# Optimization experiments

Measured on AMD Instinct MI355X. Metric: run time of the kernel, lower is better.

## Reference

```python
import jax, jax.numpy as jnp
import numpy as np

N_NODES = 50000
N_EDGES = 800000
IN_CH = 128
HID = 64
HEADS = 2
OUT_CH = 64
NEG_SLOPE = 0.2  # PyG GATv2Conv default


def setup_inputs() -> dict:
    key = jax.random.key(0)
    ks = jax.random.split(key, 16)
    x = jax.random.normal(ks[0], (N_NODES, IN_CH), dtype=jnp.float32)
    edge_index = jax.random.randint(ks[1], (2, N_EDGES), 0, N_NODES, dtype=jnp.int64)

    def glorot(k, shape):
        fan_in = shape[0]
        return jax.random.normal(k, shape, dtype=jnp.float32) / np.float32(np.sqrt(fan_in))

    # layer 1: in=128 -> heads=2, ch=64 (concat -> 128)
    # layer 2: in=128 -> heads=2, ch=64 (concat -> 128)
    # layer 3: in=128 -> heads=1, ch=64
    return {
        "x": x,
        "edge_index": edge_index,
        "W1l": glorot(ks[2], (IN_CH, HEADS * HID)),
        "W1r": glorot(ks[3], (IN_CH, HEADS * HID)),
        "att1": glorot(ks[4], (HEADS, HID)),
        "b1": jnp.zeros((HEADS * HID,), jnp.float32),
        "W2l": glorot(ks[5], (HEADS * HID, HEADS * HID)),
        "W2r": glorot(ks[6], (HEADS * HID, HEADS * HID)),
        "att2": glorot(ks[7], (HEADS, HID)),
        "b2": jnp.zeros((HEADS * HID,), jnp.float32),
        "W3l": glorot(ks[8], (HEADS * HID, OUT_CH)),
        "W3r": glorot(ks[9], (HEADS * HID, OUT_CH)),
        "att3": glorot(ks[10], (1, OUT_CH)),
        "b3": jnp.zeros((OUT_CH,), jnp.float32),
    }


def gatv2_conv(x, src, dst, Wl, Wr, att, bias, heads, ch):
    """One GATv2Conv layer (concat=True, self-loops already in src/dst)."""
    n = x.shape[0]
    xl = (x @ Wl).reshape(n, heads, ch)  # source-side transform (messages)
    xr = (x @ Wr).reshape(n, heads, ch)  # target-side transform
    # edge-wise GATv2 scoring: a^T LeakyReLU(xl_j + xr_i)
    e = jax.nn.leaky_relu(xl[src] + xr[dst], NEG_SLOPE)      # [E, H, C]
    logits = jnp.einsum('ehc,hc->eh', e, att)                 # [E, H]
    # segment softmax over incoming edges of each destination node
    amax = jax.ops.segment_max(logits, dst, num_segments=n)   # [N, H]
    ex = jnp.exp(logits - amax[dst])
    denom = jax.ops.segment_sum(ex, dst, num_segments=n)
    alpha = ex / denom[dst]                                   # [E, H]
    out = jax.ops.segment_sum(xl[src] * alpha[:, :, None], dst, num_segments=n)
    return out.reshape(n, heads * ch) + bias


def reference(x, edge_index, W1l, W1r, att1, b1, W2l, W2r, att2, b2, W3l, W3r, att3, b3):
    n = x.shape[0]
    loops = jnp.arange(n, dtype=edge_index.dtype)
    src = jnp.concatenate([edge_index[0], loops])  # add_self_loops=True
    dst = jnp.concatenate([edge_index[1], loops])
    h = jax.nn.elu(gatv2_conv(x, src, dst, W1l, W1r, att1, b1, HEADS, HID))
    h = jax.nn.elu(gatv2_conv(h, src, dst, W2l, W2r, att2, b2, HEADS, HID))
    h = jax.nn.elu(gatv2_conv(h, src, dst, W3l, W3r, att3, b3, 1, OUT_CH))
    return h
```

## Files before the change

### kernel.cpp

```cpp
#include <hip/hip_runtime.h>
#include <hip/hip_fp16.h>
#include <math.h>

#define N_NODES 50000
#define N_EDGES 800000
#define NEG_SLOPE 0.2f

#define BKT_SHIFT 7
#define N_BKT 512
#define NB_CSR ((N_NODES + 127) / 128)
#define CHUNK 2048
#define BCAP 4096
#define PB_CAP 4096
#define G1_BLOCKS (((N_NODES + 127) / 128) * 2)

typedef _Float16 v8h __attribute__((ext_vector_type(8)));
typedef _Float16 h4  __attribute__((ext_vector_type(4)));
typedef _Float16 h2  __attribute__((ext_vector_type(2)));
typedef float f32x4 __attribute__((ext_vector_type(4)));
typedef float f32x2 __attribute__((ext_vector_type(2)));

static inline int cdiv(long long a, int b) { return (int)((a + b - 1) / b); }

template<int CTRL>
static __device__ __forceinline__ float dpp_xadd(float s) {
    int t = __builtin_amdgcn_mov_dpp(__builtin_bit_cast(int, s), CTRL, 0xf, 0xf, true);
    return s + __builtin_bit_cast(float, t);
}

__global__ void pack_weights_zero(const float* __restrict__ W1l, const float* __restrict__ W1r,
                                  const float* __restrict__ W2l, const float* __restrict__ W2r,
                                  const float* __restrict__ W3l, const float* __restrict__ W3r,
                                  _Float16* __restrict__ Wt1, _Float16* __restrict__ Wt2,
                                  _Float16* __restrict__ Wt3, int* __restrict__ bcnt) {
    int id = blockIdx.x * blockDim.x + threadIdx.x;
    if (id < 32768) {
        int n = id >> 7, k = id & 127;
        Wt1[id] = (_Float16)(n < 128 ? W1l[k * 128 + n] : W1r[k * 128 + n - 128]);
    } else if (id < 65536) {
        int j = id - 32768; int n = j >> 7, k = j & 127;
        Wt2[j] = (_Float16)(n < 128 ? W2l[k * 128 + n] : W2r[k * 128 + n - 128]);
    } else if (id < 81920) {
        int j = id - 65536; int n = j >> 7, k = j & 127;
        Wt3[j] = (_Float16)(n < 64 ? W3l[k * 64 + n] : W3r[k * 64 + n - 64]);
    } else if (id < 81920 + N_BKT) {
        bcnt[id - 81920] = 0;
    }
}

__global__ __launch_bounds__(512) void bucket_scatter(const int* __restrict__ esrc,
                                                      const int* __restrict__ edst,
                                                      int* __restrict__ bcnt,
                                                      int2* __restrict__ tmp) {
    __shared__ int lhist[N_BKT];
    __shared__ int lscan[N_BKT];
    __shared__ int lofs[N_BKT];
    __shared__ int lcur[N_BKT];
    __shared__ int gbase[N_BKT];
    __shared__ int2 lpair[CHUNK];
    int tid = threadIdx.x;
    int base_e = blockIdx.x * CHUNK;
    int count = min(CHUNK, N_EDGES - base_e);

    if (tid < N_BKT) lhist[tid] = 0;
    __syncthreads();

    int e0 = base_e + tid * 4;
    int4 s4 = {0, 0, 0, 0}, d4 = {0, 0, 0, 0};
    int nmine = 0;
    if (e0 + 3 < N_EDGES && e0 + 3 < base_e + count) {
        s4 = *(const int4*)(esrc + e0);
        d4 = *(const int4*)(edst + e0);
        nmine = 4;
    } else if (e0 < N_EDGES) {
        nmine = min(N_EDGES - e0, 4);
        const int* sp = esrc + e0;
        const int* dp = edst + e0;
        if (nmine > 0) { s4.x = sp[0]; d4.x = dp[0]; }
        if (nmine > 1) { s4.y = sp[1]; d4.y = dp[1]; }
        if (nmine > 2) { s4.z = sp[2]; d4.z = dp[2]; }
    }
    int ds[4] = {d4.x, d4.y, d4.z, d4.w};
    int ss[4] = {s4.x, s4.y, s4.z, s4.w};
#pragma unroll
    for (int u = 0; u < 4; ++u)
        if (u < nmine) atomicAdd(&lhist[ds[u] >> BKT_SHIFT], 1);
    __syncthreads();

    int v = lhist[tid];
    lscan[tid] = v;
    __syncthreads();
    for (int st = 1; st < N_BKT; st <<= 1) {
        int t = (tid >= st) ? lscan[tid - st] : 0;
        __syncthreads();
        lscan[tid] += t;
        __syncthreads();
    }
    {
        int excl = lscan[tid] - v;
        lofs[tid] = excl;
        lcur[tid] = excl;
        if (v > 0) gbase[tid] = tid * BCAP + atomicAdd(&bcnt[tid], v);
    }
    __syncthreads();

#pragma unroll
    for (int u = 0; u < 4; ++u)
        if (u < nmine) {
            int b = ds[u] >> BKT_SHIFT;
            int p = atomicAdd(&lcur[b], 1);
            lpair[p] = make_int2(ss[u], ds[u]);
        }
    __syncthreads();

    for (int j = tid; j < count; j += 512) {
        int2 pr = lpair[j];
        int b = pr.y >> BKT_SHIFT;
        int idx = gbase[b] + (j - lofs[b]);
        if (idx < (b + 1) * BCAP) tmp[idx] = pr;
    }
}

__global__ __launch_bounds__(256, 2) void csr_and_gemm1(const int* __restrict__ bcnt,
                                                        const int2* __restrict__ tmp,
                                                        int* __restrict__ off,
                                                        int* __restrict__ csr,
                                                        const float* __restrict__ A,
                                                        const _Float16* __restrict__ Bt,
                                                        _Float16* __restrict__ C) {
    __shared__ int red[256];
    __shared__ int lcnt[128];
    __shared__ int sc[128];
    __shared__ int loff[129];
    __shared__ int lcur[128];
    __shared__ int lcsr[PB_CAP];
    int tid = threadIdx.x;

    if (blockIdx.x >= NB_CSR) {
        int gb = blockIdx.x - NB_CSR;
        int bx = gb >> 1;
        int by = gb & 1;
        int w = tid >> 6, lane = tid & 63;
        int m0 = bx * 128 + (w & 1) * 64;
        int n0 = by * 128 + (w >> 1) * 64;
        int q = lane >> 4, li = lane & 15;
        f32x4 acc[4][4] = {};
        const float* Ap[4];
#pragma unroll
        for (int a = 0; a < 4; ++a) {
            int row = m0 + 16 * a + li;
            if (row > N_NODES - 1) row = N_NODES - 1;
            Ap[a] = A + (size_t)row * 128 + q * 8;
        }
        const _Float16* Bp = Bt + (size_t)(n0 + li) * 128 + q * 8;
#pragma unroll
        for (int kt = 0; kt < 4; ++kt) {
            v8h af[4], bf[4];
#pragma unroll
            for (int a = 0; a < 4; ++a) {
                float4 lo = *(const float4*)(Ap[a] + kt * 32);
                float4 hi = *(const float4*)(Ap[a] + kt * 32 + 4);
                v8h t;
                t[0] = (_Float16)lo.x; t[1] = (_Float16)lo.y; t[2] = (_Float16)lo.z; t[3] = (_Float16)lo.w;
                t[4] = (_Float16)hi.x; t[5] = (_Float16)hi.y; t[6] = (_Float16)hi.z; t[7] = (_Float16)hi.w;
                af[a] = t;
            }
#pragma unroll
            for (int b = 0; b < 4; ++b) bf[b] = *(const v8h*)(Bp + (size_t)(16 * b) * 128 + kt * 32);
#pragma unroll
            for (int a = 0; a < 4; ++a)
#pragma unroll
                for (int b = 0; b < 4; ++b)
                    acc[a][b] = __builtin_amdgcn_mfma_f32_16x16x32_f16(bf[b], af[a], acc[a][b], 0, 0, 0);
        }
#pragma unroll
        for (int a = 0; a < 4; ++a) {
            int m = m0 + 16 * a + li;
            if (m < N_NODES) {
#pragma unroll
                for (int b = 0; b < 4; ++b) {
                    h4 t;
                    t[0] = (_Float16)acc[a][b][0]; t[1] = (_Float16)acc[a][b][1];
                    t[2] = (_Float16)acc[a][b][2]; t[3] = (_Float16)acc[a][b][3];
                    *(h4*)(C + (size_t)m * 256 + n0 + 16 * b + 4 * q) = t;
                }
            }
        }
        return;
    }

    int b = blockIdx.x;
    int d0 = b << BKT_SHIFT;
    int dend = min(d0 + 128, N_NODES);
    int nn = dend - d0;

    int pre = 0;
    for (int i = tid; i < b; i += 256) pre += bcnt[i];
    red[tid] = pre;
    __syncthreads();
    for (int st = 128; st > 0; st >>= 1) {
        if (tid < st) red[tid] += red[tid + st];
        __syncthreads();
    }
    int base = red[0];
    __syncthreads();

    int n = min(bcnt[b], BCAP);
    int tbase = b * BCAP;

    if (tid < 128) lcnt[tid] = 0;
    __syncthreads();
    for (int j = tid; j < n; j += 256) {
        int dl = tmp[tbase + j].y - d0;
        atomicAdd(&lcnt[dl], 1);
    }
    __syncthreads();

    if (tid < 128) sc[tid] = lcnt[tid];
    __syncthreads();
    for (int st = 1; st < 128; st <<= 1) {
        int t = (tid < 128 && tid >= st) ? sc[tid - st] : 0;
        __syncthreads();
        if (tid < 128) sc[tid] += t;
        __syncthreads();
    }
    if (tid < 128) loff[tid + 1] = sc[tid];
    if (tid == 0) loff[0] = 0;
    if (tid < 128) lcur[tid] = 0;
    __syncthreads();

    if (tid < nn) off[d0 + tid] = base + loff[tid];
    if (tid == 0 && dend == N_NODES) off[N_NODES] = base + loff[nn];

    for (int j = tid; j < n; j += 256) {
        int2 pr = tmp[tbase + j];
        int dl = pr.y - d0;
        int r = atomicAdd(&lcur[dl], 1);
        int pos = loff[dl] + r;
        if (pos < PB_CAP) lcsr[pos] = pr.x;
    }
    __syncthreads();
    for (int j = tid; j < n; j += 256) csr[base + j] = lcsr[j];
}

template<int NT>
__global__ __launch_bounds__(256, 4) void gemm_xlr(const _Float16* __restrict__ A,
                                                   const _Float16* __restrict__ Bt,
                                                   _Float16* __restrict__ C) {
    constexpr int NY = NT / 128;
    int bx = blockIdx.x / NY;
    int by = blockIdx.x % NY;
    int w = threadIdx.x >> 6, lane = threadIdx.x & 63;
    int m0 = bx * 128 + (w & 1) * 64;
    int n0 = by * 128 + (w >> 1) * 64;
    int q = lane >> 4, li = lane & 15;
    f32x4 acc[4][4] = {};
    const _Float16* Ap[4];
#pragma unroll
    for (int a = 0; a < 4; ++a) {
        int row = m0 + 16 * a + li;
        if (row > N_NODES - 1) row = N_NODES - 1;
        Ap[a] = A + (size_t)row * 128 + q * 8;
    }
    const _Float16* Bp = Bt + (size_t)(n0 + li) * 128 + q * 8;
#pragma unroll
    for (int kt = 0; kt < 4; ++kt) {
        v8h af[4], bf[4];
#pragma unroll
        for (int a = 0; a < 4; ++a) af[a] = *(const v8h*)(Ap[a] + kt * 32);
#pragma unroll
        for (int b = 0; b < 4; ++b) bf[b] = *(const v8h*)(Bp + (size_t)(16 * b) * 128 + kt * 32);
#pragma unroll
        for (int a = 0; a < 4; ++a)
#pragma unroll
            for (int b = 0; b < 4; ++b)
                acc[a][b] = __builtin_amdgcn_mfma_f32_16x16x32_f16(bf[b], af[a], acc[a][b], 0, 0, 0);
    }
#pragma unroll
    for (int a = 0; a < 4; ++a) {
        int m = m0 + 16 * a + li;
        if (m < N_NODES) {
#pragma unroll
            for (int b = 0; b < 4; ++b) {
                h4 t;
                t[0] = (_Float16)acc[a][b][0]; t[1] = (_Float16)acc[a][b][1];
                t[2] = (_Float16)acc[a][b][2]; t[3] = (_Float16)acc[a][b][3];
                *(h4*)(C + (size_t)m * NT + n0 + 16 * b + 4 * q) = t;
            }
        }
    }
}

template<int HOUT, typename OUT_T>
__global__ __launch_bounds__(256, 8) void fused_gat(
    const _Float16* __restrict__ XLR,
    const int* __restrict__ off, const int* __restrict__ csr,
    const float* __restrict__ att, const float* __restrict__ bias,
    OUT_T* __restrict__ out) {
    constexpr int VEC = 8;
    constexpr int LPE = HOUT / VEC;
    constexpr int EPW = 64 / LPE;
    constexpr int ST = 2 * HOUT;
    int wave = threadIdx.x >> 6, lane = threadIdx.x & 63;
    int node = blockIdx.x * (blockDim.x >> 6) + wave;
    if (node >= N_NODES) return;
    int g = lane / LPE;
    int lg = lane % LPE;
    int cb = lg * VEC;

    constexpr float LOG2E = 1.44269504088896340736f;
    f32x2 at2[4], xr2[4];
#pragma unroll
    for (int j = 0; j < 4; ++j) {
        at2[j][0] = att[cb + 2 * j] * LOG2E;
        at2[j][1] = att[cb + 2 * j + 1] * LOG2E;
    }
    v8h xrh = *(const v8h*)(XLR + (size_t)node * ST + HOUT + cb);
    {
        const h2* x2 = (const h2*)&xrh;
#pragma unroll
        for (int j = 0; j < 4; ++j) { xr2[j][0] = (float)x2[j][0]; xr2[j][1] = (float)x2[j][1]; }
    }

    int eoff = off[node];
    int P = off[node + 1] - eoff + 1;
    float denom = 0.f;
    f32x2 acc2[4] = {};

    const int* cp = csr + eoff;
    const _Float16* Xcb = XLR + cb;
    int pmax_i = P - 2;

    auto cidx = [&](int pos) -> int {
        int i = pos - 1;
        i = i > pmax_i ? pmax_i : i;
        return i < 0 ? 0 : i;
    };
    auto rowload = [&](int s) -> v8h {
        s = s < 0 ? 0 : s;
        s = s > N_NODES - 1 ? N_NODES - 1 : s;
        return *(const v8h*)(Xcb + (size_t)s * ST);
    };

    int p = g;
    int i1  = cp[cidx(p + EPW)];
    int i2  = cp[cidx(p + 2 * EPW)];
    int si3 = cp[cidx(p + 3 * EPW)];
    int s0  = (p == 0) ? node : cp[cidx(p)];
    v8h ah0 = rowload(s0);
    v8h ah1 = rowload(i1);
    v8h ah2 = rowload(i2);

    auto do_iter = [&](v8h& cur) {
        const h2* c2 = (const h2*)&cur;
        f32x2 a2[4];
#pragma unroll
        for (int j = 0; j < 4; ++j) { a2[j][0] = (float)c2[j][0]; a2[j][1] = (float)c2[j][1]; }
        cur = rowload(si3);
        si3 = cp[cidx(p + 4 * EPW)];

        f32x2 sdot = {0.f, 0.f};
#pragma unroll
        for (int j = 0; j < 4; ++j) {
            f32x2 v = a2[j] + xr2[j];
            f32x2 vn = v * NEG_SLOPE;
            f32x2 lv;
            lv[0] = fmaxf(v[0], vn[0]); lv[1] = fmaxf(v[1], vn[1]);
            sdot += at2[j] * lv;
        }
        float s = sdot[0] + sdot[1];
        s = dpp_xadd<0xB1>(s);
        s = dpp_xadd<0x4E>(s);
        s = dpp_xadd<0x141>(s);
        float f = exp2f(s);
        denom += f;
        f32x2 f2 = {f, f};
#pragma unroll
        for (int j = 0; j < 4; ++j) acc2[j] += a2[j] * f2;
        p += EPW;
    };

    while (p < P) {
        do_iter(ah0);
        if (p >= P) break;
        do_iter(ah1);
        if (p >= P) break;
        do_iter(ah2);
    }
#pragma unroll
    for (int o = LPE; o < 64; o <<= 1) {
#pragma unroll
        for (int j = 0; j < 4; ++j) {
            acc2[j][0] += __shfl_xor(acc2[j][0], o);
            acc2[j][1] += __shfl_xor(acc2[j][1], o);
        }
        denom += __shfl_xor(denom, o);
    }
    if (lane < LPE) {
        float inv = __builtin_amdgcn_rcpf(denom);
        OUT_T* orow = out + (size_t)node * HOUT + cb;
#pragma unroll
        for (int j = 0; j < 4; ++j) {
#pragma unroll
            for (int t = 0; t < 2; ++t) {
                float r = acc2[j][t] * inv + bias[cb + 2 * j + t];
                r = r > 0.f ? r : (__expf(r) - 1.f);
                orow[2 * j + t] = (OUT_T)r;
            }
        }
    }
}

extern "C" void kernel_launch(void* const* d_in, const int* in_sizes, int n_in,
                              void* d_out, int out_size, void* d_ws, size_t ws_size,
                              hipStream_t stream) {
    const float* x    = (const float*)d_in[0];
    const int*   ei   = (const int*)d_in[1];
    const int*   esrc = ei;
    const int*   edst = ei + N_EDGES;
    const float* W1l = (const float*)d_in[2];
    const float* W1r = (const float*)d_in[3];
    const float* att1= (const float*)d_in[4];
    const float* b1  = (const float*)d_in[5];
    const float* W2l = (const float*)d_in[6];
    const float* W2r = (const float*)d_in[7];
    const float* att2= (const float*)d_in[8];
    const float* b2  = (const float*)d_in[9];
    const float* W3l = (const float*)d_in[10];
    const float* W3r = (const float*)d_in[11];
    const float* att3= (const float*)d_in[12];
    const float* b3  = (const float*)d_in[13];
    float* out = (float*)d_out;

    _Float16* XLR = (_Float16*)d_ws;
    _Float16* Hb  = XLR + (size_t)N_NODES * 256;
    _Float16* Wt1 = Hb + (size_t)N_NODES * 128;
    _Float16* Wt2 = Wt1 + 256 * 128;
    _Float16* Wt3 = Wt2 + 256 * 128;
    int* bcnt = (int*)(Wt3 + 128 * 128);
    int* off  = bcnt + N_BKT;
    int* csr  = off + N_NODES + 1 + 1;
    int2* tmp = (int2*)(csr + N_EDGES);

    const int TB = 256;

    pack_weights_zero<<<cdiv(81920 + N_BKT, TB), TB, 0, stream>>>(
        W1l, W1r, W2l, W2r, W3l, W3r, Wt1, Wt2, Wt3, bcnt);
    bucket_scatter<<<cdiv(N_EDGES, CHUNK), 512, 0, stream>>>(esrc, edst, bcnt, tmp);
    csr_and_gemm1<<<NB_CSR + G1_BLOCKS, 256, 0, stream>>>(bcnt, tmp, off, csr, x, Wt1, XLR);

    const int WPB = 2;
    int gat_grid = cdiv(N_NODES, WPB);
    dim3 g2(cdiv(N_NODES, 128) * 2), g1(cdiv(N_NODES, 128));

    fused_gat<128, _Float16><<<gat_grid, WPB * 64, 0, stream>>>(XLR, off, csr, att1, b1, Hb);
    gemm_xlr<256><<<g2, 256, 0, stream>>>(Hb, Wt2, XLR);
    fused_gat<128, _Float16><<<gat_grid, WPB * 64, 0, stream>>>(XLR, off, csr, att2, b2, Hb);
    gemm_xlr<128><<<g1, 256, 0, stream>>>(Hb, Wt3, XLR);
    fused_gat<64, float><<<gat_grid, WPB * 64, 0, stream>>>(XLR, off, csr, att3, b3, out);
}
```

Before: 286.7 us.

## Make GAT aggregation persistent with cross-node prefetch of next node's edges

The fused GAT kernel becomes a grid-stride persistent kernel with 3072 blocks of two waves. Each wave prefetches the next node's offsets, target row and first three neighbor rows while finishing the current node, and loads offsets for the node after that. This hides the per-node startup latency of fetching offsets, CSR indices and rows. The trade-offs are higher register pressure (launch bounds changed to 128x6, and the gemm to 3 blocks per CU) and possible load imbalance from the static node assignment.

After: 425.6 us. +48.5%, slower.

```diff
diff --git a/kernel.cpp b/kernel.cpp
--- a/kernel.cpp
+++ b/kernel.cpp
@@ -244,7 +244,7 @@
 }
 
 template<int NT>
-__global__ __launch_bounds__(256, 4) void gemm_xlr(const _Float16* __restrict__ A,
+__global__ __launch_bounds__(256, 3) void gemm_xlr(const _Float16* __restrict__ A,
                                                    const _Float16* __restrict__ Bt,
                                                    _Float16* __restrict__ C) {
     constexpr int NY = NT / 128;
@@ -292,7 +292,7 @@
 }
 
 template<int HOUT, typename OUT_T>
-__global__ __launch_bounds__(256, 8) void fused_gat(
+__global__ __launch_bounds__(128, 6) void fused_gat(
     const _Float16* __restrict__ XLR,
     const int* __restrict__ off, const int* __restrict__ csr,
     const float* __restrict__ att, const float* __restrict__ bias,
@@ -302,38 +302,25 @@
     constexpr int EPW = 64 / LPE;
     constexpr int ST = 2 * HOUT;
     int wave = threadIdx.x >> 6, lane = threadIdx.x & 63;
-    int node = blockIdx.x * (blockDim.x >> 6) + wave;
-    if (node >= N_NODES) return;
+    int wid = blockIdx.x * (blockDim.x >> 6) + wave;
+    int NW = gridDim.x * (blockDim.x >> 6);
     int g = lane / LPE;
     int lg = lane % LPE;
     int cb = lg * VEC;
 
     constexpr float LOG2E = 1.44269504088896340736f;
-    f32x2 at2[4], xr2[4];
+    f32x2 at2[4];
 #pragma unroll
     for (int j = 0; j < 4; ++j) {
         at2[j][0] = att[cb + 2 * j] * LOG2E;
         at2[j][1] = att[cb + 2 * j + 1] * LOG2E;
     }
-    v8h xrh = *(const v8h*)(XLR + (size_t)node * ST + HOUT + cb);
-    {
-        const h2* x2 = (const h2*)&xrh;
-#pragma unroll
-        for (int j = 0; j < 4; ++j) { xr2[j][0] = (float)x2[j][0]; xr2[j][1] = (float)x2[j][1]; }
-    }
-
-    int eoff = off[node];
-    int P = off[node + 1] - eoff + 1;
-    float denom = 0.f;
-    f32x2 acc2[4] = {};
-
-    const int* cp = csr + eoff;
+
     const _Float16* Xcb = XLR + cb;
-    int pmax_i = P - 2;
-
-    auto cidx = [&](int pos) -> int {
+
+    auto cidx = [](int pos, int pm) -> int {
         int i = pos - 1;
-        i = i > pmax_i ? pmax_i : i;
+        i = i > pm ? pm : i;
         return i < 0 ? 0 : i;
     };
     auto rowload = [&](int s) -> v8h {
@@ -342,72 +329,131 @@
         return *(const v8h*)(Xcb + (size_t)s * ST);
     };
 
-    int p = g;
-    int i1  = cp[cidx(p + EPW)];
-    int i2  = cp[cidx(p + 2 * EPW)];
-    int si3 = cp[cidx(p + 3 * EPW)];
-    int s0  = (p == 0) ? node : cp[cidx(p)];
-    v8h ah0 = rowload(s0);
-    v8h ah1 = rowload(i1);
-    v8h ah2 = rowload(i2);
-
-    auto do_iter = [&](v8h& cur) {
-        const h2* c2 = (const h2*)&cur;
-        f32x2 a2[4];
-#pragma unroll
-        for (int j = 0; j < 4; ++j) { a2[j][0] = (float)c2[j][0]; a2[j][1] = (float)c2[j][1]; }
-        cur = rowload(si3);
-        si3 = cp[cidx(p + 4 * EPW)];
-
-        f32x2 sdot = {0.f, 0.f};
-#pragma unroll
-        for (int j = 0; j < 4; ++j) {
-            f32x2 v = a2[j] + xr2[j];
-            f32x2 vn = v * NEG_SLOPE;
-            f32x2 lv;
-            lv[0] = fmaxf(v[0], vn[0]); lv[1] = fmaxf(v[1], vn[1]);
-            sdot += at2[j] * lv;
-        }
-        float s = sdot[0] + sdot[1];
-        s = dpp_xadd<0xB1>(s);
-        s = dpp_xadd<0x4E>(s);
-        s = dpp_xadd<0x141>(s);
-        float f = exp2f(s);
-        denom += f;
-        f32x2 f2 = {f, f};
-#pragma unroll
-        for (int j = 0; j < 4; ++j) acc2[j] += a2[j] * f2;
-        p += EPW;
-    };
-
-    while (p < P) {
-        do_iter(ah0);
-        if (p >= P) break;
-        do_iter(ah1);
-        if (p >= P) break;
-        do_iter(ah2);
-    }
-#pragma unroll
-    for (int o = LPE; o < 64; o <<= 1) {
-#pragma unroll
-        for (int j = 0; j < 4; ++j) {
-            acc2[j][0] += __shfl_xor(acc2[j][0], o);
-            acc2[j][1] += __shfl_xor(acc2[j][1], o);
-        }
-        denom += __shfl_xor(denom, o);
-    }
-    if (lane < LPE) {
-        float inv = __builtin_amdgcn_rcpf(denom);
-        OUT_T* orow = out + (size_t)node * HOUT + cb;
-#pragma unroll
-        for (int j = 0; j < 4; ++j) {
-#pragma unroll
-            for (int t = 0; t < 2; ++t) {
-                float r = acc2[j][t] * inv + bias[cb + 2 * j + t];
-                r = r > 0.f ? r : (__expf(r) - 1.f);
-                orow[2 * j + t] = (OUT_T)r;
+    int node = wid;
+    if (node >= N_NODES) return;
+
+    int eoff = off[node], eend = off[node + 1];
+    v8h xrh = *(const v8h*)(XLR + (size_t)node * ST + HOUT + cb);
+    int P = eend - eoff + 1;
+    const int* cp = csr + eoff;
+    int pmax = P - 2;
+    int si3 = cp[cidx(g + 3 * EPW, pmax)];
+    int s0c = (g == 0) ? node : cp[cidx(g, pmax)];
+    v8h ah0 = rowload(s0c);
+    v8h ah1 = rowload(cp[cidx(g + EPW, pmax)]);
+    v8h ah2 = rowload(cp[cidx(g + 2 * EPW, pmax)]);
+
+    int nnode = node + NW;
+    int n_eoff = 0, n_eend = 0;
+    v8h n_xrh = {};
+    if (nnode < N_NODES) {
+        n_eoff = off[nnode]; n_eend = off[nnode + 1];
+        n_xrh = *(const v8h*)(XLR + (size_t)nnode * ST + HOUT + cb);
+    }
+
+    while (true) {
+        int n2 = node + 2 * NW;
+        int a_eoff = 0, a_eend = 0;
+        v8h a_xrh = {};
+        if (n2 < N_NODES) {
+            a_eoff = off[n2]; a_eend = off[n2 + 1];
+            a_xrh = *(const v8h*)(XLR + (size_t)n2 * ST + HOUT + cb);
+        }
+
+        f32x2 xr2[4];
+        {
+            const h2* x2 = (const h2*)&xrh;
+#pragma unroll
+            for (int j = 0; j < 4; ++j) { xr2[j][0] = (float)x2[j][0]; xr2[j][1] = (float)x2[j][1]; }
+        }
+
+        bool has_next = nnode < N_NODES;
+        int n_pmax = 0, n_si3 = 0, n_s0 = 0, n_i1 = 0, n_i2 = 0;
+        const int* ncp = nullptr;
+        if (has_next) {
+            int nP = n_eend - n_eoff + 1;
+            ncp = csr + n_eoff;
+            n_pmax = nP - 2;
+            n_s0 = (g == 0) ? nnode : ncp[cidx(g, n_pmax)];
+            n_i1 = ncp[cidx(g + EPW, n_pmax)];
+            n_i2 = ncp[cidx(g + 2 * EPW, n_pmax)];
+            n_si3 = ncp[cidx(g + 3 * EPW, n_pmax)];
+        }
+
+        float denom = 0.f;
+        f32x2 acc2[4] = {};
+        int p = g;
+        auto do_iter = [&](v8h& curv) {
+            const h2* c2 = (const h2*)&curv;
+            f32x2 a2[4];
+#pragma unroll
+            for (int j = 0; j < 4; ++j) { a2[j][0] = (float)c2[j][0]; a2[j][1] = (float)c2[j][1]; }
+            curv = rowload(si3);
+            si3 = cp[cidx(p + 4 * EPW, pmax)];
+
+            f32x2 sdot = {0.f, 0.f};
+#pragma unroll
+            for (int j = 0; j < 4; ++j) {
+                f32x2 v = a2[j] + xr2[j];
+                f32x2 vn = v * NEG_SLOPE;
+                f32x2 lv;
+                lv[0] = fmaxf(v[0], vn[0]); lv[1] = fmaxf(v[1], vn[1]);
+                sdot += at2[j] * lv;
             }
-        }
+            float s = sdot[0] + sdot[1];
+            s = dpp_xadd<0xB1>(s);
+            s = dpp_xadd<0x4E>(s);
+            s = dpp_xadd<0x141>(s);
+            float f = exp2f(s);
+            denom += f;
+            f32x2 f2 = {f, f};
+#pragma unroll
+            for (int j = 0; j < 4; ++j) acc2[j] += a2[j] * f2;
+            p += EPW;
+        };
+        while (p < P) {
+            do_iter(ah0);
+            if (p >= P) break;
+            do_iter(ah1);
+            if (p >= P) break;
+            do_iter(ah2);
+        }
+
+        if (has_next) {
+            ah0 = rowload(n_s0);
+            ah1 = rowload(n_i1);
+            ah2 = rowload(n_i2);
+        }
+
+#pragma unroll
+        for (int o = LPE; o < 64; o <<= 1) {
+#pragma unroll
+            for (int j = 0; j < 4; ++j) {
+                acc2[j][0] += __shfl_xor(acc2[j][0], o);
+                acc2[j][1] += __shfl_xor(acc2[j][1], o);
+            }
+            denom += __shfl_xor(denom, o);
+        }
+        if (lane < LPE) {
+            float inv = __builtin_amdgcn_rcpf(denom);
+            OUT_T* orow = out + (size_t)node * HOUT + cb;
+#pragma unroll
+            for (int j = 0; j < 4; ++j) {
+#pragma unroll
+                for (int t = 0; t < 2; ++t) {
+                    float r = acc2[j][t] * inv + bias[cb + 2 * j + t];
+                    r = r > 0.f ? r : (__expf(r) - 1.f);
+                    orow[2 * j + t] = (OUT_T)r;
+                }
+            }
+        }
+        if (!has_next) return;
+
+        node = nnode; nnode = n2;
+        eoff = n_eoff; eend = n_eend; xrh = n_xrh;
+        P = eend - eoff + 1;
+        cp = ncp; pmax = n_pmax; si3 = n_si3;
+        n_eoff = a_eoff; n_eend = a_eend; n_xrh = a_xrh;
     }
 }
 
@@ -449,13 +495,12 @@
     bucket_scatter<<<cdiv(N_EDGES, CHUNK), 512, 0, stream>>>(esrc, edst, bcnt, tmp);
     csr_and_gemm1<<<NB_CSR + G1_BLOCKS, 256, 0, stream>>>(bcnt, tmp, off, csr, x, Wt1, XLR);
 
-    const int WPB = 2;
-    int gat_grid = cdiv(N_NODES, WPB);
+    const int GAT_BLOCKS = 3072;
     dim3 g2(cdiv(N_NODES, 128) * 2), g1(cdiv(N_NODES, 128));
 
-    fused_gat<128, _Float16><<<gat_grid, WPB * 64, 0, stream>>>(XLR, off, csr, att1, b1, Hb);
+    fused_gat<128, _Float16><<<GAT_BLOCKS, 128, 0, stream>>>(XLR, off, csr, att1, b1, Hb);
     gemm_xlr<256><<<g2, 256, 0, stream>>>(Hb, Wt2, XLR);
-    fused_gat<128, _Float16><<<gat_grid, WPB * 64, 0, stream>>>(XLR, off, csr, att2, b2, Hb);
+    fused_gat<128, _Float16><<<GAT_BLOCKS, 128, 0, stream>>>(XLR, off, csr, att2, b2, Hb);
     gemm_xlr<128><<<g1, 256, 0, stream>>>(Hb, Wt3, XLR);
-    fused_gat<64, float><<<gat_grid, WPB * 64, 0, stream>>>(XLR, off, csr, att3, b3, out);
-}
+    fused_gat<64, float><<<GAT_BLOCKS, 128, 0, stream>>>(XLR, off, csr, att3, b3, out);
+}
```
